# Performance work log

Hardware: AMD Instinct MI355X
Metric: run time of the kernel (lower is better)

## Reference

```python
import jax, jax.numpy as jnp
import numpy as np

NUM_HEADS = 8
WS1, WS2 = 3, 5
SR = 8
RES = 56
DIM = 256


def _normalize(x, axis=-1, eps=1e-12):
    n = jnp.linalg.norm(x, axis=axis, keepdims=True)
    return x / jnp.maximum(n, eps)


def _unfold(img, ws):
    # img: (B, C, H, W) -> (B, C, ws*ws, H*W), torch nn.Unfold ordering
    B, C, H, W = img.shape
    p = ws // 2
    pad = jnp.pad(img, ((0, 0), (0, 0), (p, p), (p, p)))
    cols = jnp.stack([pad[:, :, i:i + H, j:j + W]
                      for i in range(ws) for j in range(ws)], axis=2)
    return cols.reshape(B, C, ws * ws, H * W)


def _local_mask(H, W, ws):
    # True where the unfolded window position falls on zero padding; shape (N, ws*ws)
    ones = jnp.ones((1, 1, H, W), jnp.float32)
    cols = _unfold(ones, ws)[0, 0]            # (ws*ws, N)
    return cols.T == 0                         # (N, ws*ws)


def _layernorm(x, g, b, eps=1e-5):
    mu = x.mean(-1, keepdims=True)
    var = ((x - mu) ** 2).mean(-1, keepdims=True)
    return (x - mu) * jax.lax.rsqrt(var + eps) * g + b


def setup_inputs() -> dict:
    key = jax.random.key(0)
    ks = jax.random.split(key, 8)
    C, B, N = DIM, 4, RES * RES
    hd = C // NUM_HEADS

    def nrm(k, shape, s=0.02):
        return jax.random.normal(k, shape, jnp.float32) * s

    return {
        "x": jax.random.normal(ks[0], (B, N, C), jnp.float32),
        "Wq": nrm(ks[1], (C, C)), "bq": jnp.zeros((C,), jnp.float32),
        "Wkv": nrm(ks[2], (C, 2 * C)), "bkv": jnp.zeros((2 * C,), jnp.float32),
        "Wsr": nrm(ks[3], (C, C)), "bsr": jnp.zeros((C,), jnp.float32),
        "ln_g": jnp.ones((C,), jnp.float32), "ln_b": jnp.zeros((C,), jnp.float32),
        "tok1": nrm(ks[4], (NUM_HEADS, hd, WS1 * WS1)),
        "bias1": jnp.zeros((NUM_HEADS, 1, WS1 * WS1), jnp.float32),
        "tok2": nrm(ks[5], (NUM_HEADS, hd, WS2 * WS2)),
        "bias2": jnp.zeros((NUM_HEADS, 1, WS2 * WS2), jnp.float32),
        "Wproj": nrm(ks[6], (C, C)), "bproj": jnp.zeros((C,), jnp.float32),
        "patch_size": 56,
    }


def reference(x, Wq, bq, Wkv, bkv, Wsr, bsr, ln_g, ln_b,
              tok1, bias1, tok2, bias2, Wproj, bproj, patch_size):
    H = W = int(patch_size)
    B, N, C = x.shape
    h = NUM_HEADS
    d = C // h
    l1, l2 = WS1 * WS1, WS2 * WS2

    # queries, cosine-normalized per head
    q = (x @ Wq + bq).reshape(B, N, h, d).transpose(0, 2, 1, 3)   # (B,h,N,d)
    qn = _normalize(q)

    # shared kv projection (torch computes it twice with identical result)
    kv = x @ Wkv + bkv
    k, v = kv[..., :C], kv[..., C:]
    kn = _normalize(k.reshape(B, N, h, d)).reshape(B, N, C)
    kv_img = jnp.concatenate([kn, v], axis=-1).transpose(0, 2, 1).reshape(B, 2 * C, H, W)

    def local_branch(ws):
        l = ws * ws
        cols = _unfold(kv_img, ws)                                # (B,2C,l,N)
        cols = cols.reshape(B, 2 * h, d, l, N).transpose(0, 1, 4, 2, 3)  # (B,2h,N,d,l)
        kl, vl = cols[:, :h], cols[:, h:]
        a = jnp.einsum('bhnd,bhndl->bhnl', qn, kl)
        a = jnp.where(_local_mask(H, W, ws)[None, None], -jnp.inf, a)
        return a, vl

    a1, vl1 = local_branch(WS1)
    a2, vl2 = local_branch(WS2)

    # pooled global branch
    x_img = x.transpose(0, 2, 1).reshape(B, C, H, W)
    x_sr = jnp.einsum('bchw,oc->bohw', x_img, Wsr.T.T) if False else jnp.einsum('bchw,co->bohw', x_img, Wsr) + bsr[None, :, None, None]
    x_sr = jax.nn.gelu(x_sr, approximate=False)
    pH, pW = H // SR, W // SR
    pooled = x_sr.reshape(B, C, pH, SR, pW, SR).mean(axis=(3, 5))  # adaptive avg pool
    P = pH * pW
    x_p = pooled.reshape(B, C, P).transpose(0, 2, 1)               # (B,P,C)
    x_p = _layernorm(x_p, ln_g, ln_b)
    kvp = (x_p @ Wkv + bkv).reshape(B, P, 2 * h, d).transpose(0, 2, 1, 3)
    kp, vp = kvp[:, :h], kvp[:, h:]
    ap = jnp.einsum('bhnd,bhpd->bhnp', qn, _normalize(kp))

    # joint softmax over both local windows and pooled tokens
    attn = jax.nn.softmax(jnp.concatenate([a1, a2, ap], axis=-1), axis=-1)
    s1 = attn[..., :l1]
    s2 = attn[..., l1:l1 + l2]
    sp = attn[..., l1 + l2:]

    x1 = jnp.einsum('bhnl,bhndl->bhnd',
                    jnp.einsum('bhnd,hdl->bhnl', qn, tok1) + bias1[None] + s1, vl1)
    x2 = jnp.einsum('bhnl,bhndl->bhnd',
                    jnp.einsum('bhnd,hdl->bhnl', qn, tok2) + bias2[None] + s2, vl2)
    xp = jnp.einsum('bhnp,bhpd->bhnd', sp, vp)

    out = (x1 + x2 + xp).transpose(0, 2, 1, 3).reshape(B, N, C)
    return out @ Wproj + bproj
```

## Files before the change

kernel.cpp:

```cpp
#include <hip/hip_runtime.h>
#include <hip/hip_bf16.h>

using bf16 = __hip_bfloat16;

#define B_  4
#define H_  56
#define W_  56
#define N_  3136
#define C_  256
#define NH  8
#define HD  32
#define P_  49
#define PH  7
#define TOKC 272
#define KS2  136
#define CPAD 80
#define VTH  60
#define VTW  64

typedef __attribute__((ext_vector_type(8))) short short8;
typedef __attribute__((ext_vector_type(4))) float f32x4;

union U8 { uint4 u; short8 s; };

__device__ __forceinline__ float bfu2f(ushort u) { return __uint_as_float((uint32_t)u << 16); }
__device__ __forceinline__ ushort f2bf_u(float f) {
    uint32_t u = __float_as_uint(f);
    uint32_t r = (u + 0x7FFFu + ((u >> 16) & 1u)) >> 16;
    return (ushort)r;
}
__device__ __forceinline__ uint32_t pk2(float a, float b) {
    return (uint32_t)f2bf_u(a) | ((uint32_t)f2bf_u(b) << 16);
}
__device__ __forceinline__ float lo16(uint32_t u) { return __uint_as_float(u << 16); }
__device__ __forceinline__ float hi16(uint32_t u) { return __uint_as_float(u & 0xffff0000u); }

__device__ __forceinline__ float half_reduce(float v) {
#pragma unroll
    for (int m = 16; m >= 1; m >>= 1) v += __shfl_xor(v, m);
    return v;
}

__device__ __forceinline__ float block_sum(float val, float* red) {
#pragma unroll
    for (int m = 32; m >= 1; m >>= 1) val += __shfl_xor(val, m);
    __syncthreads();
    if ((threadIdx.x & 63) == 0) red[threadIdx.x >> 6] = val;
    __syncthreads();
    return red[0] + red[1] + red[2] + red[3];
}

__global__ __launch_bounds__(256) void k_prep(
    const float* __restrict__ Wq, const float* __restrict__ Wkv,
    const float* __restrict__ Wsr, const float* __restrict__ Wproj,
    const float* __restrict__ tok1, const float* __restrict__ bias1,
    const float* __restrict__ tok2, const float* __restrict__ bias2,
    ushort* __restrict__ WT, ushort* __restrict__ WTp,
    ushort* __restrict__ TD, float* __restrict__ biasT,
    ushort* __restrict__ vT, uint32_t* __restrict__ vpT32)
{
    const int gid = blockIdx.x * 256 + threadIdx.x;
    const int gs = gridDim.x * 256;
    for (int i = gid; i < 1024 * 256; i += gs) {
        int o = i >> 8, c = i & 255;
        float w = (o < 256) ? Wq[c * 256 + o]
                : (o < 768) ? Wkv[c * 512 + (o - 256)]
                            : Wsr[c * 256 + (o - 768)];
        WT[i] = f2bf_u(w);
    }
    for (int i = gid; i < 256 * 256; i += gs) {
        int o = i >> 8, c = i & 255;
        WTp[i] = f2bf_u(Wproj[c * 256 + o]);
    }
    for (int i = gid; i < 320 * 256; i += gs) {
        int j = i >> 8, k = i & 255;
        float val = 0.f;
        if (j < TOKC) {
            int h = j / 34, l = j % 34;
            if ((k >> 5) == h) {
                int d = k & 31;
                val = (l < 9) ? tok1[(h * HD + d) * 9 + l]
                              : tok2[(h * HD + d) * 25 + (l - 9)];
            }
        }
        TD[i] = f2bf_u(val);
    }
    for (int i = gid; i < 320; i += gs) {
        float bv = 0.f;
        if (i < TOKC) {
            int h = i / 34, l = i % 34;
            bv = (l < 9) ? bias1[h * 9 + l] : bias2[h * 25 + (l - 9)];
        }
        biasT[i] = bv;
    }
    const int nimg = B_ * 256;
    for (int i = gid; i < nimg * 704; i += gs) {
        int img = i / 704, c = i % 704;
        int y, x;
        if (c < 256) { int yi = c >> 6; y = (yi < 2) ? yi : yi + 56; x = c & 63; }
        else { int cc = c - 256; y = 2 + cc / 8; int xx = cc % 8; x = (xx < 2) ? xx : xx + 56; }
        vT[(size_t)img * VTH * VTW + y * VTW + x] = 0;
    }
    for (int i = gid; i < B_ * 256 * 32; i += gs) vpT32[i] = 0u;
}

__global__ __launch_bounds__(256) void k_gemm_in(
    const float* __restrict__ xf,
    const ushort* __restrict__ WT,
    const float* __restrict__ bq, const float* __restrict__ bkv,
    const float* __restrict__ bsr,
    ushort* __restrict__ qnu,
    ushort* __restrict__ knu, ushort* __restrict__ vT, ushort* __restrict__ srgu)
{
    const int r0 = blockIdx.x * 64;
    const int halfy = blockIdx.y;
    const int t = threadIdx.x;
    __shared__ __align__(16) ushort As[64 * 264];
    __shared__ __align__(16) ushort Bs[64 * 264];

#pragma unroll
    for (int i = 0; i < 8; i++) {
        int chunk = t + i * 256;
        int row = chunk >> 5, ks8 = (chunk & 31) * 8;
        const float* src = xf + (size_t)(r0 + row) * 256 + ks8;
        float4 f0 = *(const float4*)(src);
        float4 f1 = *(const float4*)(src + 4);
        uint4 o;
        o.x = pk2(f0.x, f0.y); o.y = pk2(f0.z, f0.w);
        o.z = pk2(f1.x, f1.y); o.w = pk2(f1.z, f1.w);
        *(uint4*)(As + row * 264 + ks8) = o;
    }
    __syncthreads();

    const int w = t >> 6, lane = t & 63;
    const int arow = w * 16 + (lane & 15);
    const int k0 = (lane >> 4) * 8;
    const int colq = lane & 15;
    const int rb = r0 + w * 16 + (lane >> 4) * 4;

    short8 areg[8];
#pragma unroll
    for (int kk = 0; kk < 8; kk++)
        areg[kk] = *(const short8*)(As + arow * 264 + kk * 32 + k0);

    for (int cc = 0; cc < 8; cc++) {
        const int cb = halfy * 512 + cc * 64;
        const int mode = cb >> 8;
        const int cm = cb & 255;

        __syncthreads();
#pragma unroll
        for (int i = 0; i < 8; i++) {
            int chunk = t + i * 256;
            int row = chunk >> 5, ks8 = (chunk & 31) * 8;
            *(uint4*)(Bs + row * 264 + ks8) =
                *(const uint4*)(WT + (size_t)(cb + row) * 256 + ks8);
        }
        __syncthreads();

        f32x4 acc[4];
#pragma unroll
        for (int ct = 0; ct < 4; ct++) acc[ct] = (f32x4){0.f, 0.f, 0.f, 0.f};
#pragma unroll
        for (int kk = 0; kk < 8; kk++) {
#pragma unroll
            for (int ct = 0; ct < 4; ct++) {
                short8 b = *(const short8*)(Bs + (ct * 16 + colq) * 264 + kk * 32 + k0);
                acc[ct] = __builtin_amdgcn_mfma_f32_16x16x32_bf16(areg[kk], b, acc[ct], 0, 0, 0);
            }
        }

        const float* bp = (mode == 0) ? bq : (mode == 1) ? bkv : (mode == 2) ? (bkv + 256) : bsr;
#pragma unroll
        for (int ct = 0; ct < 4; ct++) {
            float bv = bp[cm + ct * 16 + colq];
#pragma unroll
            for (int j = 0; j < 4; j++) acc[ct][j] += bv;
        }

        if (mode <= 1) {
#pragma unroll
            for (int hp = 0; hp < 2; hp++) {
#pragma unroll
                for (int j = 0; j < 4; j++) {
                    float ss = acc[2 * hp][j] * acc[2 * hp][j] + acc[2 * hp + 1][j] * acc[2 * hp + 1][j];
                    ss += __shfl_xor(ss, 1); ss += __shfl_xor(ss, 2);
                    ss += __shfl_xor(ss, 4); ss += __shfl_xor(ss, 8);
                    float inv = 1.0f / fmaxf(sqrtf(ss), 1e-12f);
                    acc[2 * hp][j] *= inv; acc[2 * hp + 1][j] *= inv;
                }
            }
        } else if (mode == 3) {
#pragma unroll
            for (int ct = 0; ct < 4; ct++)
#pragma unroll
                for (int j = 0; j < 4; j++) {
                    float s = acc[ct][j];
                    acc[ct][j] = 0.5f * s * (1.0f + erff(s * 0.70710678118654752f));
                }
        }

#pragma unroll
        for (int ct = 0; ct < 4; ct++) {
            int gcol = cm + ct * 16 + colq;
#pragma unroll
            for (int j = 0; j < 4; j++) {
                float vvv = acc[ct][j];
                size_t ro = (size_t)(rb + j);
                if (mode == 0)      qnu[ro * 256 + gcol] = f2bf_u(vvv);
                else if (mode == 1) knu[ro * 256 + gcol] = f2bf_u(vvv);
                else if (mode == 2) {
                    int bb = (int)(ro / N_), n = (int)(ro % N_);
                    int yy = n / W_, xx = n % W_;
                    vT[((size_t)(bb * 256 + gcol) * VTH + yy + 2) * VTW + xx + 2] = f2bf_u(vvv);
                } else {
                    srgu[ro * 256 + gcol] = f2bf_u(vvv);
                }
            }
        }
    }
}

__global__ __launch_bounds__(256) void k_gemm_proj(
    const ushort* __restrict__ Abf,
    const ushort* __restrict__ WT,
    const float*  __restrict__ bias,
    float* __restrict__ dstF)
{
    const int r0 = blockIdx.x * 64;
    const int cb = blockIdx.y * 64;
    const int t = threadIdx.x;
    __shared__ __align__(16) ushort As[64 * 264];
    __shared__ __align__(16) ushort Bs[64 * 264];

#pragma unroll
    for (int i = 0; i < 8; i++) {
        int chunk = t + i * 256;
        int row = chunk >> 5, ks = (chunk & 31) * 8;
        *(uint4*)(As + row * 264 + ks) = *(const uint4*)(Abf + (size_t)(r0 + row) * 256 + ks);
        *(uint4*)(Bs + row * 264 + ks) = *(const uint4*)(WT + (size_t)(cb + row) * 256 + ks);
    }
    __syncthreads();

    const int w = t >> 6, lane = t & 63;
    const int arow = w * 16 + (lane & 15);
    const int k0 = (lane >> 4) * 8;
    f32x4 acc[4];
#pragma unroll
    for (int ct = 0; ct < 4; ct++) acc[ct] = (f32x4){0.f, 0.f, 0.f, 0.f};

#pragma unroll
    for (int kk = 0; kk < 8; kk++) {
        short8 a = *(const short8*)(As + arow * 264 + kk * 32 + k0);
#pragma unroll
        for (int ct = 0; ct < 4; ct++) {
            short8 b = *(const short8*)(Bs + (ct * 16 + (lane & 15)) * 264 + kk * 32 + k0);
            acc[ct] = __builtin_amdgcn_mfma_f32_16x16x32_bf16(a, b, acc[ct], 0, 0, 0);
        }
    }

    const int colq = lane & 15;
    const int rb = r0 + w * 16 + (lane >> 4) * 4;
#pragma unroll
    for (int ct = 0; ct < 4; ct++) {
        float bv = bias[cb + ct * 16 + colq];
#pragma unroll
        for (int j = 0; j < 4; j++) acc[ct][j] += bv;
    }

#pragma unroll
    for (int ct = 0; ct < 4; ct++) {
        int gcol = cb + ct * 16 + colq;
#pragma unroll
        for (int j = 0; j < 4; j++)
            dstF[(size_t)(rb + j) * 256 + gcol] = acc[ct][j];
    }
}

__global__ __launch_bounds__(256) void k_srt(
    const uint32_t* __restrict__ srgu32,
    const float* __restrict__ Wkv, const float* __restrict__ bkv,
    const float* __restrict__ ln_g, const float* __restrict__ ln_b,
    ushort* __restrict__ kpn_u, ushort* __restrict__ vpT)
{
    const int cell = blockIdx.x;
    const int b = cell / P_, p = cell % P_;
    const int py = p / PH, px = p % PH;
    const int t = threadIdx.x;
    const int ph = t >> 7, cp = t & 127;
    __shared__ float xp[C_];
    __shared__ float red[4];

    float sx = 0.f, sy = 0.f;
    for (int k = 0; k < 32; k++) {
        int pi = ph * 32 + k;
        int n = (py * 8 + (pi >> 3)) * W_ + px * 8 + (pi & 7);
        uint32_t u = srgu32[((size_t)b * N_ + n) * 128 + cp];
        sx += lo16(u); sy += hi16(u);
    }
    if (ph == 1) { xp[2 * cp] = sx; xp[2 * cp + 1] = sy; }
    __syncthreads();
    if (ph == 0) {
        xp[2 * cp]     = (xp[2 * cp] + sx) * (1.0f / 64.0f);
        xp[2 * cp + 1] = (xp[2 * cp + 1] + sy) * (1.0f / 64.0f);
    }
    __syncthreads();

    float acc = xp[t];
    float mean = block_sum(acc, red) * (1.0f / C_);
    float dv = acc - mean;
    float var = block_sum(dv * dv, red) * (1.0f / C_);
    float xpv = dv * rsqrtf(var + 1e-5f) * ln_g[t] + ln_b[t];
    __syncthreads();
    xp[t] = xpv;
    __syncthreads();

    float ak = bkv[t];
    float av = bkv[C_ + t];
    for (int c = 0; c < C_; c++) {
        float xv = xp[c];
        ak += xv * Wkv[c * 2 * C_ + t];
        av += xv * Wkv[c * 2 * C_ + C_ + t];
    }
    float nk = fmaxf(sqrtf(half_reduce(ak * ak)), 1e-12f);
    kpn_u[(size_t)cell * C_ + t] = f2bf_u(ak / nk);
    vpT[((size_t)b * 256 + t) * 64 + p] = f2bf_u(av);
}

__global__ __launch_bounds__(256) void k_qkav(
    const ushort* __restrict__ qnu,
    const uint32_t* __restrict__ knu,
    const ushort* __restrict__ kpnu,
    const ushort* __restrict__ TD,
    const float* __restrict__ biasT,
    const ushort* __restrict__ vT,
    const ushort* __restrict__ vpT,
    ushort* __restrict__ preu)
{
    const int tile = blockIdx.x;
    const int b  = blockIdx.y >> 1;
    const int hs = blockIdx.y & 1;
    const int ty = tile / 14, tx = tile % 14;
    const int t = threadIdx.x;

    __shared__ __align__(16) ushort shmem[2 * 4 * 16 * CPAD];
    __shared__ ushort tokcS[16 * 136];
    ushort* ks = shmem;
    ushort* coefW = shmem;
    ushort* coefP = shmem + 4 * 16 * CPAD;

    uint32_t* ks32 = (uint32_t*)ks;
    for (int idx = t; idx < 64 * 32; idx += 256) {
        int r = idx >> 5, u2 = idx & 31;
        int gy = ty * 4 + (r >> 3) - 2, gx = tx * 4 + (r & 7) - 2;
        uint2 kv = make_uint2(0u, 0u);
        if (gy >= 0 && gy < H_ && gx >= 0 && gx < W_)
            kv = *reinterpret_cast<const uint2*>(
                knu + ((size_t)b * N_ + gy * W_ + gx) * 128 + hs * 64 + 2 * u2);
        ks32[r * (KS2 / 2) + 2 * u2]     = kv.x;
        ks32[r * (KS2 / 2) + 2 * u2 + 1] = kv.y;
    }
    __syncthreads();

    const int w = t >> 6, lane = t & 63;
    const int h = hs * 4 + w;
    const int col = lane & 15, kslc = lane >> 4;

    int r8[4], c8[4]; bool inb[4]; int pcl[4]; bool pval[4];
#pragma unroll
    for (int ct = 0; ct < 4; ct++) {
        int key = ct * 16 + col;
        r8[ct] = key >> 3; c8[ct] = key & 7;
        int gy = ty * 4 + r8[ct] - 2, gx = tx * 4 + c8[ct] - 2;
        inb[ct] = (gy >= 0) && (gy < H_) && (gx >= 0) && (gx < W_);
        pval[ct] = key < P_;
        pcl[ct] = pval[ct] ? key : (P_ - 1);
    }

    size_t aflat = (size_t)b * N_ + (ty * 4 + (col >> 2)) * W_ + tx * 4 + (col & 3);
    short8 a = *(const short8*)(qnu + aflat * 256 + h * 32 + kslc * 8);

    f32x4 aw[4], ap[4];
#pragma unroll
    for (int ct = 0; ct < 4; ct++) {
        short8 bw = *(const short8*)(ks + (ct * 16 + col) * KS2 + w * 32 + kslc * 8);
        aw[ct] = __builtin_amdgcn_mfma_f32_16x16x32_bf16(a, bw, (f32x4){0.f,0.f,0.f,0.f}, 0, 0, 0);
        short8 bp = *(const short8*)(kpnu + ((size_t)b * P_ + pcl[ct]) * 256 + h * 32 + kslc * 8);
        ap[ct] = __builtin_amdgcn_mfma_f32_16x16x32_bf16(a, bp, (f32x4){0.f,0.f,0.f,0.f}, 0, 0, 0);
    }

    f32x4 at[3];
#pragma unroll
    for (int ct = 0; ct < 3; ct++) {
        short8 bt = *(const short8*)(TD + (size_t)(h * 34 + ct * 16 + col) * 256 + h * 32 + kslc * 8);
        at[ct] = __builtin_amdgcn_mfma_f32_16x16x32_bf16(a, bt, (f32x4){0.f,0.f,0.f,0.f}, 0, 0, 0);
    }
#pragma unroll
    for (int ct = 0; ct < 3; ct++) {
        int l = ct * 16 + col;
        if (l < 34) {
            float bT = biasT[h * 34 + l];
#pragma unroll
            for (int j = 0; j < 4; j++)
                tokcS[(kslc * 4 + j) * 136 + w * 34 + l] = f2bf_u(at[ct][j] + bT);
        }
    }

    __syncthreads();

#pragma unroll
    for (int j = 0; j < 4; j++) {
        float mj = -INFINITY;
#pragma unroll
        for (int ct = 0; ct < 4; ct++) {
            int dy = r8[ct] - kslc - 2, dx = c8[ct] - j - 2;
            bool win = inb[ct] && dy >= -2 && dy <= 2 && dx >= -2 && dx <= 2;
            if (win) mj = fmaxf(mj, aw[ct][j]);
            if (pval[ct]) mj = fmaxf(mj, ap[ct][j]);
        }
        mj = fmaxf(mj, __shfl_xor(mj, 1)); mj = fmaxf(mj, __shfl_xor(mj, 2));
        mj = fmaxf(mj, __shfl_xor(mj, 4)); mj = fmaxf(mj, __shfl_xor(mj, 8));
        float ej = 0.f;
        float ew[4], ep[4];
#pragma unroll
        for (int ct = 0; ct < 4; ct++) {
            int dy = r8[ct] - kslc - 2, dx = c8[ct] - j - 2;
            bool win = inb[ct] && dy >= -2 && dy <= 2 && dx >= -2 && dx <= 2;
            bool inner = dy >= -1 && dy <= 1 && dx >= -1 && dx <= 1;
            ew[ct] = win ? (inner ? 2.0f : 1.0f) * __expf(aw[ct][j] - mj) : 0.f;
            ep[ct] = pval[ct] ? __expf(ap[ct][j] - mj) : 0.f;
            ej += ew[ct] + ep[ct];
        }
        ej += __shfl_xor(ej, 1); ej += __shfl_xor(ej, 2);
        ej += __shfl_xor(ej, 4); ej += __shfl_xor(ej, 8);
        float sc = 1.0f / ej;
        const ushort* tokc_j = tokcS + (kslc * 4 + j) * 136 + w * 34;
        const int trow = (w * 16 + kslc * 4 + j) * CPAD;
#pragma unroll
        for (int ct = 0; ct < 4; ct++) {
            int dy = r8[ct] - kslc - 2, dx = c8[ct] - j - 2;
            float cw = 0.f;
            if (dy >= -2 && dy <= 2 && dx >= -2 && dx <= 2) {
                bool inner = dy >= -1 && dy <= 1 && dx >= -1 && dx <= 1;
                int l25 = (dy + 2) * 5 + (dx + 2);
                float tm = bfu2f(tokc_j[9 + l25]);
                if (inner) tm += bfu2f(tokc_j[(dy + 1) * 3 + (dx + 1)]);
                cw = ew[ct] * sc + tm;
            }
            coefW[trow + ct * 16 + col] = f2bf_u(cw);
            coefP[trow + ct * 16 + col] = f2bf_u(pval[ct] ? ep[ct] * sc : 0.f);
        }
    }
    __syncthreads();

    f32x4 accO[2];
    accO[0] = (f32x4){0.f,0.f,0.f,0.f};
    accO[1] = (f32x4){0.f,0.f,0.f,0.f};
#pragma unroll
    for (int kc = 0; kc < 2; kc++) {
        short8 aWf = *(const short8*)(coefW + (w * 16 + col) * CPAD + kc * 32 + kslc * 8);
        short8 aPf = *(const short8*)(coefP + (w * 16 + col) * CPAD + kc * 32 + kslc * 8);
#pragma unroll
        for (int ct = 0; ct < 2; ct++) {
            int chg = hs * 128 + w * 32 + ct * 16 + col;
            size_t vbase = (((size_t)(b * 256 + chg)) * VTH + ty * 4 + kc * 4 + kslc) * VTW + tx * 4;
            uint2 l0 = *(const uint2*)(vT + vbase);
            uint2 l1 = *(const uint2*)(vT + vbase + 4);
            U8 ub; ub.u = make_uint4(l0.x, l0.y, l1.x, l1.y);
            accO[ct] = __builtin_amdgcn_mfma_f32_16x16x32_bf16(aWf, ub.s, accO[ct], 0, 0, 0);
            short8 bPf = *(const short8*)(vpT + ((size_t)b * 256 + chg) * 64 + kc * 32 + kslc * 8);
            accO[ct] = __builtin_amdgcn_mfma_f32_16x16x32_bf16(aPf, bPf, accO[ct], 0, 0, 0);
        }
    }
#pragma unroll
    for (int ct = 0; ct < 2; ct++) {
        int chg = hs * 128 + w * 32 + ct * 16 + col;
#pragma unroll
        for (int j = 0; j < 4; j++) {
            size_t pflat = (size_t)b * N_ + (ty * 4 + kslc) * W_ + tx * 4 + j;
            preu[pflat * 256 + chg] = f2bf_u(accO[ct][j]);
        }
    }
}

extern "C" void kernel_launch(void* const* d_in, const int* in_sizes, int n_in,
                              void* d_out, int out_size, void* d_ws, size_t ws_size,
                              hipStream_t stream)
{
    (void)in_sizes; (void)n_in; (void)out_size; (void)ws_size;
    const float* x     = (const float*)d_in[0];
    const float* Wq    = (const float*)d_in[1];
    const float* bq    = (const float*)d_in[2];
    const float* Wkv   = (const float*)d_in[3];
    const float* bkv   = (const float*)d_in[4];
    const float* Wsr   = (const float*)d_in[5];
    const float* bsr   = (const float*)d_in[6];
    const float* ln_g  = (const float*)d_in[7];
    const float* ln_b  = (const float*)d_in[8];
    const float* tok1  = (const float*)d_in[9];
    const float* bias1 = (const float*)d_in[10];
    const float* tok2  = (const float*)d_in[11];
    const float* bias2 = (const float*)d_in[12];
    const float* Wproj = (const float*)d_in[13];
    const float* bproj = (const float*)d_in[14];
    float* out = (float*)d_out;

    const size_t nhalf = (size_t)B_ * N_ * 128;
    const size_t nvt   = (size_t)B_ * 256 * VTH * VTW;

    uint32_t* knu    = (uint32_t*)d_ws;
    uint32_t* srgu   = knu + nhalf;
    uint32_t* qnu32  = srgu + nhalf;
    ushort*   vTus   = (ushort*)(qnu32 + nhalf);
    ushort*   WTus   = vTus + nvt;
    ushort*   WTpus  = WTus + 1024 * 256;
    ushort*   TDus   = WTpus + 256 * 256;
    float*    biasT  = (float*)(TDus + 320 * 256);
    ushort*   vpTus  = (ushort*)(biasT + 320);
    ushort*   kpnuS  = vpTus + (size_t)B_ * 256 * 64;

    ushort* qnu = (ushort*)qnu32;

    k_prep<<<512, 256, 0, stream>>>(Wq, Wkv, Wsr, Wproj, tok1, bias1, tok2, bias2,
                                    WTus, WTpus, TDus, biasT,
                                    vTus, (uint32_t*)vpTus);
    k_gemm_in<<<dim3(196, 2), 256, 0, stream>>>(x, WTus, bq, bkv, bsr,
                                                qnu, (ushort*)knu, vTus, (ushort*)srgu);
    k_srt<<<B_ * P_, 256, 0, stream>>>(srgu, Wkv, bkv, ln_g, ln_b, kpnuS, vpTus);
    k_qkav<<<dim3(196, B_ * 2), 256, 0, stream>>>(qnu, knu, kpnuS, TDus, biasT,
                                                  vTus, vpTus, (ushort*)srgu);
    k_gemm_proj<<<dim3(196, 4), 256, 0, stream>>>((ushort*)srgu, WTpus, bproj, out);
}
```

Before: 106.4 us.

## Prefetch weight tiles into registers and transpose V stores through LDS

```diff
diff --git a/kernel.cpp b/kernel.cpp
--- a/kernel.cpp
+++ b/kernel.cpp
@@ -143,6 +143,17 @@
     for (int kk = 0; kk < 8; kk++)
         areg[kk] = *(const short8*)(As + arow * 264 + kk * 32 + k0);
 
+    uint4 L[8];
+    {
+        const int cb = halfy * 512;
+#pragma unroll
+        for (int i = 0; i < 8; i++) {
+            int chunk = t + i * 256;
+            int row = chunk >> 5, ks8 = (chunk & 31) * 8;
+            L[i] = *(const uint4*)(WT + (size_t)(cb + row) * 256 + ks8);
+        }
+    }
+
     for (int cc = 0; cc < 8; cc++) {
         const int cb = halfy * 512 + cc * 64;
         const int mode = cb >> 8;
@@ -153,10 +164,19 @@
         for (int i = 0; i < 8; i++) {
             int chunk = t + i * 256;
             int row = chunk >> 5, ks8 = (chunk & 31) * 8;
-            *(uint4*)(Bs + row * 264 + ks8) =
-                *(const uint4*)(WT + (size_t)(cb + row) * 256 + ks8);
+            *(uint4*)(Bs + row * 264 + ks8) = L[i];
         }
         __syncthreads();
+
+        if (cc < 7) {
+            const int cbn = halfy * 512 + (cc + 1) * 64;
+#pragma unroll
+            for (int i = 0; i < 8; i++) {
+                int chunk = t + i * 256;
+                int row = chunk >> 5, ks8 = (chunk & 31) * 8;
+                L[i] = *(const uint4*)(WT + (size_t)(cbn + row) * 256 + ks8);
+            }
+        }
 
         f32x4 acc[4];
 #pragma unroll
@@ -200,21 +220,38 @@
                 }
         }
 
-#pragma unroll
-        for (int ct = 0; ct < 4; ct++) {
-            int gcol = cm + ct * 16 + colq;
-#pragma unroll
-            for (int j = 0; j < 4; j++) {
-                float vvv = acc[ct][j];
-                size_t ro = (size_t)(rb + j);
-                if (mode == 0)      qnu[ro * 256 + gcol] = f2bf_u(vvv);
-                else if (mode == 1) knu[ro * 256 + gcol] = f2bf_u(vvv);
-                else if (mode == 2) {
-                    int bb = (int)(ro / N_), n = (int)(ro % N_);
-                    int yy = n / W_, xx = n % W_;
-                    vT[((size_t)(bb * 256 + gcol) * VTH + yy + 2) * VTW + xx + 2] = f2bf_u(vvv);
-                } else {
-                    srgu[ro * 256 + gcol] = f2bf_u(vvv);
+        if (mode == 2) {
+#pragma unroll
+            for (int ct = 0; ct < 4; ct++) {
+#pragma unroll
+                for (int j = 0; j < 4; j++) {
+                    int tok_l = w * 16 + (lane >> 4) * 4 + j;
+                    As[(ct * 16 + colq) * 66 + tok_l] = f2bf_u(acc[ct][j]);
+                }
+            }
+            __syncthreads();
+            const int bb = r0 / N_;
+            const int n0 = r0 % N_;
+            const int tok = t & 63;
+            const int n = n0 + tok;
+            const int yy = n / W_, xx = n % W_;
+#pragma unroll
+            for (int p = 0; p < 16; p++) {
+                int ch_l = (t >> 6) * 16 + p;
+                vT[((size_t)(bb * 256 + cm + ch_l) * VTH + yy + 2) * VTW + xx + 2] =
+                    As[ch_l * 66 + tok];
+            }
+        } else {
+#pragma unroll
+            for (int ct = 0; ct < 4; ct++) {
+                int gcol = cm + ct * 16 + colq;
+#pragma unroll
+                for (int j = 0; j < 4; j++) {
+                    float vvv = acc[ct][j];
+                    size_t ro = (size_t)(rb + j);
+                    if (mode == 0)      qnu[ro * 256 + gcol] = f2bf_u(vvv);
+                    else if (mode == 1) knu[ro * 256 + gcol] = f2bf_u(vvv);
+                    else                srgu[ro * 256 + gcol] = f2bf_u(vvv);
                 }
             }
         }
@@ -456,6 +493,7 @@
     f32x4 accO[2];
     accO[0] = (f32x4){0.f,0.f,0.f,0.f};
     accO[1] = (f32x4){0.f,0.f,0.f,0.f};
+    __builtin_amdgcn_s_setprio(1);
 #pragma unroll
     for (int kc = 0; kc < 2; kc++) {
         short8 aWf = *(const short8*)(coefW + (w * 16 + col) * CPAD + kc * 32 + kslc * 8);
@@ -472,6 +510,7 @@
             accO[ct] = __builtin_amdgcn_mfma_f32_16x16x32_bf16(aPf, bPf, accO[ct], 0, 0, 0);
         }
     }
+    __builtin_amdgcn_s_setprio(0);
 #pragma unroll
     for (int ct = 0; ct < 2; ct++) {
         int chg = hs * 128 + w * 32 + ct * 16 + col;
```

Result: slower. 126.4 us (+18.8%).
